# Kernel tuning notes

Measured on AMD Instinct MI355X. Metric: run time of the kernel, lower is better.

Reference implementation:

```python
import jax, jax.numpy as jnp
import numpy as np

VOCAB = 32000
D = 512
H = 8
B = 1
SEQ = 4096
CHUNK = 1024  # max_len == chunk size


def _pe(seq, d):
    pos = np.arange(seq, dtype=np.float32)[:, None]
    div = np.exp(np.arange(0, d, 2, dtype=np.float32) * (-np.log(10000.0) / d))
    pe = np.zeros((seq, d), dtype=np.float32)
    pe[:, 0::2] = np.sin(pos * div)
    pe[:, 1::2] = np.cos(pos * div)
    return jnp.asarray(pe)


def _mha(x, w_in, b_in, w_out, b_out, h):
    # x: (..., L, d); attention along L, batched over leading dims.
    lead = x.shape[:-2]
    L, d = x.shape[-2], x.shape[-1]
    hd = d // h
    qkv = x @ w_in.T + b_in                      # (..., L, 3d)
    q, k, v = jnp.split(qkv, 3, axis=-1)
    q = q.reshape(lead + (L, h, hd))
    k = k.reshape(lead + (L, h, hd))
    v = v.reshape(lead + (L, h, hd))
    scores = jnp.einsum('...qhd,...khd->...hqk', q, k) * (1.0 / np.sqrt(hd))
    attn = jax.nn.softmax(scores, axis=-1)
    o = jnp.einsum('...hqk,...khd->...qhd', attn, v).reshape(lead + (L, d))
    return o @ w_out.T + b_out


def _ln(x, g, b, eps=1e-5):
    m = x.mean(-1, keepdims=True)
    v = x.var(-1, keepdims=True)
    return (x - m) / jnp.sqrt(v + eps) * g + b


def setup_inputs() -> dict:
    key = jax.random.key(0)
    ks = jax.random.split(key, 10)
    n = lambda k, s: jax.random.normal(k, s, jnp.float32) * 0.02
    return {
        'tokens': jax.random.randint(ks[0], (B, SEQ), 0, VOCAB),
        'emb': n(ks[1], (VOCAB, D)),
        'chunk_w_in': n(ks[2], (3 * D, D)), 'chunk_b_in': jnp.zeros((3 * D,), jnp.float32),
        'chunk_w_out': n(ks[3], (D, D)), 'chunk_b_out': jnp.zeros((D,), jnp.float32),
        'glob_w_in': n(ks[4], (3 * D, D)), 'glob_b_in': jnp.zeros((3 * D,), jnp.float32),
        'glob_w_out': n(ks[5], (D, D)), 'glob_b_out': jnp.zeros((D,), jnp.float32),
        'ln1_g': jnp.ones((D,), jnp.float32), 'ln1_b': jnp.zeros((D,), jnp.float32),
        'ffn_w1': n(ks[6], (4 * D, D)), 'ffn_b1': jnp.zeros((4 * D,), jnp.float32),
        'ffn_w2': n(ks[7], (D, 4 * D)), 'ffn_b2': jnp.zeros((D,), jnp.float32),
        'ln2_g': jnp.ones((D,), jnp.float32), 'ln2_b': jnp.zeros((D,), jnp.float32),
        'fc_w': n(ks[8], (VOCAB, D)), 'fc_b': jnp.zeros((VOCAB,), jnp.float32),
    }


def reference(tokens, emb, chunk_w_in, chunk_b_in, chunk_w_out, chunk_b_out,
              glob_w_in, glob_b_in, glob_w_out, glob_b_out,
              ln1_g, ln1_b, ffn_w1, ffn_b1, ffn_w2, ffn_b2,
              ln2_g, ln2_b, fc_w, fc_b):
    # embedding * sqrt(d) + sinusoidal positional encoding (dropout in eval = identity)
    x = emb[tokens] * np.sqrt(D).astype(np.float32) + _pe(SEQ, D)[None]  # (B, S, d)
    b, s, d = x.shape
    nc = s // CHUNK
    # BeamSplitter chunk stage: attend across the nc chunks at each intra-chunk position
    xc = x.reshape(b, nc, CHUNK, d).transpose(0, 2, 1, 3)   # (B, CHUNK, nc, d)
    ca = _mha(xc, chunk_w_in, chunk_b_in, chunk_w_out, chunk_b_out, H)
    ca = ca.transpose(0, 2, 1, 3).reshape(b, s, d)          # (B, S, d)
    # global stage: full attention over the sequence
    ga = _mha(ca, glob_w_in, glob_b_in, glob_w_out, glob_b_out, H)
    # post-norm transformer encoder layer
    x = _ln(x + ga, ln1_g, ln1_b)
    f = jax.nn.relu(x @ ffn_w1.T + ffn_b1) @ ffn_w2.T + ffn_b2
    x = _ln(x + f, ln2_g, ln2_b)
    return x @ fc_w.T + fc_b                                 # (B, S, VOCAB)
```

## Files before the change

### kernel.cpp

```cpp
#include <hip/hip_runtime.h>

typedef __attribute__((ext_vector_type(8))) short bf16x8;
typedef __attribute__((ext_vector_type(4))) float f32x4;
typedef unsigned short u16;

__device__ __forceinline__ u16 f2b(float f) {
  union { float f; unsigned u; } v; v.f = f;
  return (u16)((v.u + 0x7FFFu + ((v.u >> 16) & 1u)) >> 16);
}
__device__ __forceinline__ float b2f(u16 x) {
  union { unsigned u; float f; } v; v.u = (unsigned)x << 16; return v.f;
}

__device__ __forceinline__ void gload16(const void* g, void* l) {
  __builtin_amdgcn_global_load_lds((__attribute__((address_space(1))) void*)(g),
                                   (__attribute__((address_space(3))) void*)(l),
                                   16, 0, 0);
}

__device__ __forceinline__ void mbar() {
  asm volatile("" ::: "memory");
  __builtin_amdgcn_s_barrier();
  asm volatile("" ::: "memory");
}

__device__ __forceinline__ void cv1(const float4* __restrict__ s, u16* __restrict__ d, int i) {
  float4 v = s[i];
  unsigned long long pk = (unsigned long long)f2b(v.x) |
                          ((unsigned long long)f2b(v.y) << 16) |
                          ((unsigned long long)f2b(v.z) << 32) |
                          ((unsigned long long)f2b(v.w) << 48);
  *(unsigned long long*)(d + (size_t)i * 4) = pk;
}

__global__ __launch_bounds__(256)
void prep(const int* __restrict__ tok, const float* __restrict__ emb,
          float* __restrict__ xf, u16* __restrict__ xb,
          const float4* s0, u16* d0, const float4* s1, u16* d1,
          const float4* s2, u16* d2, const float4* s3, u16* d3,
          const float4* s4, u16* d4, const float4* s5, u16* d5,
          const float4* s6, u16* d6) {
  if (blockIdx.x < 4096) {
    const int s = blockIdx.x;
    const int i = threadIdx.x;
    const int t = tok[s];
    const float div = __expf((float)(2 * i) * -0.017988946039015984f);
    const float ang = (float)s * div;
    const float sv = __sinf(ang), cv = __cosf(ang);
    const float* e = emb + (size_t)t * 512 + 2 * i;
    const float x0 = e[0] * 22.627416997969522f + sv;
    const float x1 = e[1] * 22.627416997969522f + cv;
    const size_t o = (size_t)s * 512 + 2 * i;
    xf[o] = x0; xf[o + 1] = x1;
    xb[o] = f2b(x0); xb[o + 1] = f2b(x1);
    return;
  }
  int i = (blockIdx.x - 4096) * 256 + threadIdx.x;
  const int stride = ((int)gridDim.x - 4096) * 256;
  for (; i < 5144576; i += stride) {
    int j = i;
    if (j < 196608) { cv1(s0, d0, j); continue; }
    j -= 196608;
    if (j < 65536) { cv1(s1, d1, j); continue; }
    j -= 65536;
    if (j < 196608) { cv1(s2, d2, j); continue; }
    j -= 196608;
    if (j < 65536) { cv1(s3, d3, j); continue; }
    j -= 65536;
    if (j < 262144) { cv1(s4, d4, j); continue; }
    j -= 262144;
    if (j < 262144) { cv1(s5, d5, j); continue; }
    j -= 262144;
    cv1(s6, d6, j);
  }
}

template<int BM, int BN, int RELU, int WF32, int WB16>
__global__ __launch_bounds__(256)
void gemm_bt(const u16* __restrict__ A, const u16* __restrict__ B,
             const float* __restrict__ bias, float* __restrict__ Cf,
             u16* __restrict__ Cb, int M, int N, int K)
{
  constexpr int MFR = BM / 32;
  constexpr int NFR = BN / 32;
  constexpr int INFLT = BM / 32 + BN / 32;
  __shared__ __align__(16) u16 As[2][BM * 64];
  __shared__ __align__(16) u16 Bs[2][BN * 64];
  const int tid = threadIdx.x;
  const int wid = tid >> 6, lane = tid & 63;
  const int lo = lane & 15, hi = lane >> 4;
  const int nbn = N / BN;
  const int cpx = (int)gridDim.x >> 3;
  const int bid = blockIdx.x;
  const int swz = (bid & 7) * cpx + (bid >> 3);
  const int bi = swz / nbn, bj = swz - bi * nbn;
  const size_t row0 = (size_t)bi * BM, col0 = (size_t)bj * BN;
  const int wr = (wid >> 1) * (BM / 2), wc = (wid & 1) * (BN / 2);
  const int srow = (wid << 3) + (lane >> 3);
  const int scol = ((lane & 7) ^ (lane >> 3)) << 3;

  f32x4 acc[MFR][NFR] = {};

  auto stage = [&](int t, int b) {
    const int k0 = t << 6;
#pragma unroll
    for (int p = 0; p < BM / 32; ++p)
      gload16(A + (row0 + srow + 32 * p) * (size_t)K + k0 + scol, &As[b][(wid * 8 + 32 * p) * 64]);
#pragma unroll
    for (int p = 0; p < BN / 32; ++p)
      gload16(B + (col0 + srow + 32 * p) * (size_t)K + k0 + scol, &Bs[b][(wid * 8 + 32 * p) * 64]);
  };

  auto rdf = [&](const u16* base, int row, int ks) -> bf16x8 {
    return *(const bf16x8*)((const char*)base + row * 128 + ((((ks << 2) | hi) ^ (row & 7)) << 4));
  };

  const int T = K >> 6;
  stage(0, 0);
  stage(1, 1);

  for (int t = 0; t < T; ++t) {
    if (t + 1 < T) {
      if constexpr (INFLT == 4)      { asm volatile("s_waitcnt vmcnt(4)" ::: "memory"); }
      else if constexpr (INFLT == 6) { asm volatile("s_waitcnt vmcnt(6)" ::: "memory"); }
      else                           { asm volatile("s_waitcnt vmcnt(8)" ::: "memory"); }
    } else {
      asm volatile("s_waitcnt vmcnt(0)" ::: "memory");
    }
    __builtin_amdgcn_sched_barrier(0);
    mbar();
    const u16* Ab = As[t & 1];
    const u16* Bb = Bs[t & 1];
#pragma unroll
    for (int ks = 0; ks < 2; ++ks) {
      bf16x8 af[MFR], bfr[NFR];
#pragma unroll
      for (int m = 0; m < MFR; ++m) af[m] = rdf(Ab, wr + m * 16 + lo, ks);
#pragma unroll
      for (int n = 0; n < NFR; ++n) bfr[n] = rdf(Bb, wc + n * 16 + lo, ks);
#pragma unroll
      for (int m = 0; m < MFR; ++m)
#pragma unroll
        for (int n = 0; n < NFR; ++n)
          acc[m][n] = __builtin_amdgcn_mfma_f32_16x16x32_bf16(af[m], bfr[n], acc[m][n], 0, 0, 0);
    }
    mbar();
    if (t + 2 < T) stage(t + 2, t & 1);
  }

#pragma unroll
  for (int m = 0; m < MFR; ++m)
#pragma unroll
    for (int n = 0; n < NFR; ++n) {
      const size_t c = col0 + wc + n * 16 + lo;
      const float bv = bias[c];
#pragma unroll
      for (int i = 0; i < 4; ++i) {
        const size_t r = row0 + wr + m * 16 + hi * 4 + i;
        float v = acc[m][n][i] + bv;
        if (RELU) v = fmaxf(v, 0.0f);
        if (WF32) Cf[r * (size_t)N + c] = v;
        if (WB16) Cb[r * (size_t)N + c] = f2b(v);
      }
    }
}

template<int KC>
__global__ __launch_bounds__(512, 2)
void gemm256(const u16* __restrict__ A, const u16* __restrict__ B,
             const float* __restrict__ bias, float* __restrict__ C,
             int M, int N)
{
  constexpr int T = KC / 64;
  __shared__ __align__(16) u16 LA[2][256 * 64];
  __shared__ __align__(16) u16 LB[2][256 * 64];
  const int tid = threadIdx.x;
  const int wid = tid >> 6, lane = tid & 63;
  const int lo = lane & 15, hi = lane >> 4;
  const int nbn = N >> 8;
  const int cpx = (int)gridDim.x >> 3;
  const int bid = blockIdx.x;
  const int swz = (bid & 7) * cpx + (bid >> 3);
  const int bi = swz / nbn, bj = swz - bi * nbn;
  const size_t row0 = (size_t)bi << 8, col0 = (size_t)bj << 8;
  const int wrow = (wid >> 2) << 7;
  const int wcol = (wid & 3) << 6;

  const int srow = (wid << 3) + (lane >> 3);
  const int scol = ((lane & 7) ^ (lane >> 3)) << 3;
  const u16* srcA = A + (row0 + srow) * (size_t)KC + scol;
  const u16* srcB = B + (col0 + srow) * (size_t)KC + scol;
  const int ldst = wid << 9;

  f32x4 acc[8][4] = {};

  auto stage = [&](int t, int b) {
    const size_t ko = (size_t)t * 64;
#pragma unroll
    for (int i = 0; i < 4; ++i)
      gload16(srcA + ko + (size_t)(i * 64) * KC, &LA[b][ldst + i * 4096]);
#pragma unroll
    for (int i = 0; i < 4; ++i)
      gload16(srcB + ko + (size_t)(i * 64) * KC, &LB[b][ldst + i * 4096]);
  };

  auto rd = [&](const u16* base, int row, int ks) -> bf16x8 {
    const int byte = row * 128 + ((((ks << 2) | hi) ^ (row & 7)) << 4);
    return *(const bf16x8*)((const char*)base + byte);
  };

  auto storeHalf = [&](int mbase) {
#pragma unroll
    for (int m = 0; m < 4; ++m)
#pragma unroll
      for (int n = 0; n < 4; ++n) {
        const size_t c = col0 + wcol + n * 16 + lo;
        const float bv = bias[c];
#pragma unroll
        for (int i = 0; i < 4; ++i) {
          const size_t r = row0 + wrow + (mbase + m) * 16 + hi * 4 + i;
          __builtin_nontemporal_store(acc[mbase + m][n][i] + bv, &C[r * (size_t)N + c]);
        }
      }
  };

  stage(0, 0);
  stage(1, 1);

  for (int t = 0; t < T - 1; ++t) {
    const int b = t & 1;
    const u16* Ab = LA[b];
    const u16* Bb = LB[b];
    asm volatile("s_waitcnt vmcnt(8)" ::: "memory");
    __builtin_amdgcn_sched_barrier(0);
    mbar();

    bf16x8 afr[4], bfr[4];
#pragma unroll
    for (int ks = 0; ks < 2; ++ks) {
#pragma unroll
      for (int m = 0; m < 4; ++m) afr[m] = rd(Ab, wrow + m * 16 + lo, ks);
#pragma unroll
      for (int n = 0; n < 4; ++n) bfr[n] = rd(Bb, wcol + n * 16 + lo, ks);
      mbar();
      asm volatile("s_waitcnt lgkmcnt(0)" ::: "memory");
      __builtin_amdgcn_sched_barrier(0);
      __builtin_amdgcn_s_setprio(1);
#pragma unroll
      for (int m = 0; m < 4; ++m)
#pragma unroll
        for (int n = 0; n < 4; ++n)
          acc[m][n] = __builtin_amdgcn_mfma_f32_16x16x32_bf16(afr[m], bfr[n], acc[m][n], 0, 0, 0);
      __builtin_amdgcn_s_setprio(0);
      mbar();
#pragma unroll
      for (int m = 0; m < 4; ++m) afr[m] = rd(Ab, wrow + (4 + m) * 16 + lo, ks);
      mbar();
      asm volatile("s_waitcnt lgkmcnt(0)" ::: "memory");
      __builtin_amdgcn_sched_barrier(0);
      __builtin_amdgcn_s_setprio(1);
#pragma unroll
      for (int m = 0; m < 4; ++m)
#pragma unroll
        for (int n = 0; n < 4; ++n)
          acc[4 + m][n] = __builtin_amdgcn_mfma_f32_16x16x32_bf16(afr[m], bfr[n], acc[4 + m][n], 0, 0, 0);
      __builtin_amdgcn_s_setprio(0);
      mbar();
    }
    if (t + 2 < T) stage(t + 2, b);
  }

  {
    const u16* Ab = LA[(T - 1) & 1];
    const u16* Bb = LB[(T - 1) & 1];
    asm volatile("s_waitcnt vmcnt(0)" ::: "memory");
    __builtin_amdgcn_sched_barrier(0);
    mbar();

    bf16x8 afr[4], bfr[4];
#pragma unroll
    for (int m = 0; m < 4; ++m) afr[m] = rd(Ab, wrow + m * 16 + lo, 0);
#pragma unroll
    for (int n = 0; n < 4; ++n) bfr[n] = rd(Bb, wcol + n * 16 + lo, 0);
    mbar();
    asm volatile("s_waitcnt lgkmcnt(0)" ::: "memory");
    __builtin_amdgcn_sched_barrier(0);
#pragma unroll
    for (int m = 0; m < 4; ++m)
#pragma unroll
      for (int n = 0; n < 4; ++n)
        acc[m][n] = __builtin_amdgcn_mfma_f32_16x16x32_bf16(afr[m], bfr[n], acc[m][n], 0, 0, 0);
    mbar();
#pragma unroll
    for (int m = 0; m < 4; ++m) afr[m] = rd(Ab, wrow + (4 + m) * 16 + lo, 0);
    mbar();
    asm volatile("s_waitcnt lgkmcnt(0)" ::: "memory");
    __builtin_amdgcn_sched_barrier(0);
#pragma unroll
    for (int m = 0; m < 4; ++m)
#pragma unroll
      for (int n = 0; n < 4; ++n)
        acc[4 + m][n] = __builtin_amdgcn_mfma_f32_16x16x32_bf16(afr[m], bfr[n], acc[4 + m][n], 0, 0, 0);
    mbar();
#pragma unroll
    for (int m = 0; m < 4; ++m) afr[m] = rd(Ab, wrow + m * 16 + lo, 1);
#pragma unroll
    for (int n = 0; n < 4; ++n) bfr[n] = rd(Bb, wcol + n * 16 + lo, 1);
    asm volatile("s_waitcnt lgkmcnt(0)" ::: "memory");
    __builtin_amdgcn_sched_barrier(0);
#pragma unroll
    for (int m = 0; m < 4; ++m)
#pragma unroll
      for (int n = 0; n < 4; ++n)
        acc[m][n] = __builtin_amdgcn_mfma_f32_16x16x32_bf16(afr[m], bfr[n], acc[m][n], 0, 0, 0);
    storeHalf(0);
#pragma unroll
    for (int m = 0; m < 4; ++m) afr[m] = rd(Ab, wrow + (4 + m) * 16 + lo, 1);
    asm volatile("s_waitcnt lgkmcnt(0)" ::: "memory");
    __builtin_amdgcn_sched_barrier(0);
#pragma unroll
    for (int m = 0; m < 4; ++m)
#pragma unroll
      for (int n = 0; n < 4; ++n)
        acc[4 + m][n] = __builtin_amdgcn_mfma_f32_16x16x32_bf16(afr[m], bfr[n], acc[4 + m][n], 0, 0, 0);
    storeHalf(4);
  }
}

__global__ __launch_bounds__(256)
void chunk_attn(const u16* __restrict__ qkv, u16* __restrict__ out) {
  const int widx = threadIdx.x >> 6, d = threadIdx.x & 63;
  const int g = blockIdx.x * 4 + widx;
  const int p = g & 1023, h = g >> 10;
  float q[4], k[4], v[4];
#pragma unroll
  for (int c = 0; c < 4; ++c) {
    const u16* b = qkv + (size_t)((c << 10) + p) * 1536 + (h << 6) + d;
    q[c] = b2f(b[0]); k[c] = b2f(b[512]); v[c] = b2f(b[1024]);
  }
  float sc[4][4];
#pragma unroll
  for (int i = 0; i < 4; ++i)
#pragma unroll
    for (int j = 0; j < 4; ++j) sc[i][j] = q[i] * k[j];
#pragma unroll
  for (int mask = 1; mask < 64; mask <<= 1)
#pragma unroll
    for (int i = 0; i < 4; ++i)
#pragma unroll
      for (int j = 0; j < 4; ++j) sc[i][j] += __shfl_xor(sc[i][j], mask);
#pragma unroll
  for (int i = 0; i < 4; ++i) {
    float s0 = sc[i][0] * 0.125f, s1 = sc[i][1] * 0.125f,
          s2 = sc[i][2] * 0.125f, s3 = sc[i][3] * 0.125f;
    const float mx = fmaxf(fmaxf(s0, s1), fmaxf(s2, s3));
    const float e0 = __expf(s0 - mx), e1 = __expf(s1 - mx),
                e2 = __expf(s2 - mx), e3 = __expf(s3 - mx);
    const float inv = 1.0f / (e0 + e1 + e2 + e3);
    const float o = (e0 * v[0] + e1 * v[1] + e2 * v[2] + e3 * v[3]) * inv;
    out[(size_t)((i << 10) + p) * 512 + (h << 6) + d] = f2b(o);
  }
}

__global__ __launch_bounds__(512, 4)
void flash_attn(const u16* __restrict__ qkv, float* __restrict__ pO,
                float* __restrict__ pm, float* __restrict__ pl) {
  __shared__ __align__(16) u16 Ks[64 * 64];
  __shared__ __align__(16) u16 Vt[64 * 64];
  __shared__ __align__(16) u16 Pp[8][16 * 64];
  const int tid = threadIdx.x, wid = tid >> 6, lane = tid & 63;
  const int lo = lane & 15, hi = lane >> 4;
  const int q0 = blockIdx.x << 7, h = blockIdx.y, z = blockIdx.z;
  const int kvb = z << 11;
  const int hoff = h << 6;
  char* KsB = (char*)Ks; char* VtB = (char*)Vt;
  char* Pw = (char*)&Pp[wid][0];
  const int xsw = (lo & 7) << 4;
  constexpr float C1 = 0.18033688011112042f;

  bf16x8 qf[2];
#pragma unroll
  for (int kh = 0; kh < 2; ++kh)
    qf[kh] = *(const bf16x8*)(qkv + (size_t)(q0 + wid * 16 + lo) * 1536 + hoff + kh * 32 + hi * 8);

  f32x4 o[4] = {};
  float mr = -3e38f, lr = 0.f;

  const int krow = tid >> 3, kq = tid & 7;

  bf16x8 kpre = *(const bf16x8*)(qkv + (size_t)(kvb + krow) * 1536 + 512 + hoff + kq * 8);
  bf16x8 vpre = *(const bf16x8*)(qkv + (size_t)(kvb + krow) * 1536 + 1024 + hoff + kq * 8);

  for (int kv0 = kvb; kv0 < kvb + 2048; kv0 += 64) {
    __syncthreads();
    *(bf16x8*)(KsB + ((krow * 128 + kq * 16) ^ ((krow & 7) << 4))) = kpre;
    {
      const unsigned* vp = (const unsigned*)&vpre;
      const int oddr = krow & 1;
      const unsigned t0 = oddr ? vp[0] : vp[2];
      const unsigned t1 = oddr ? vp[1] : vp[3];
      const unsigned r0 = (unsigned)__shfl_xor((int)t0, 8);
      const unsigned r1 = (unsigned)__shfl_xor((int)t1, 8);
      const unsigned E0 = oddr ? r0 : vp[0];
      const unsigned E1 = oddr ? r1 : vp[1];
      const unsigned O0 = oddr ? vp[2] : r0;
      const unsigned O1 = oddr ? vp[3] : r1;
      const int jp = krow & ~1;
      const int db = kq * 8 + oddr * 4;
      unsigned w0 = (E0 & 0xffffu) | (O0 << 16);
      unsigned w1 = (E0 >> 16) | (O0 & 0xffff0000u);
      unsigned w2 = (E1 & 0xffffu) | (O1 << 16);
      unsigned w3 = (E1 >> 16) | (O1 & 0xffff0000u);
      *(unsigned*)(VtB + (((db + 0) * 128 + 2 * jp) ^ (((db + 0) & 7) << 4))) = w0;
      *(unsigned*)(VtB + (((db + 1) * 128 + 2 * jp) ^ (((db + 1) & 7) << 4))) = w1;
      *(unsigned*)(VtB + (((db + 2) * 128 + 2 * jp) ^ (((db + 2) & 7) << 4))) = w2;
      *(unsigned*)(VtB + (((db + 3) * 128 + 2 * jp) ^ (((db + 3) & 7) << 4))) = w3;
    }
    __syncthreads();
    if (kv0 + 64 < kvb + 2048) {
      kpre = *(const bf16x8*)(qkv + (size_t)(kv0 + 64 + krow) * 1536 + 512 + hoff + kq * 8);
      vpre = *(const bf16x8*)(qkv + (size_t)(kv0 + 64 + krow) * 1536 + 1024 + hoff + kq * 8);
    }

    f32x4 s[4] = {};
#pragma unroll
    for (int n = 0; n < 4; ++n) {
      const int key = n * 16 + lo;
#pragma unroll
      for (int kh = 0; kh < 2; ++kh) {
        bf16x8 kf = *(const bf16x8*)(KsB + ((key * 128 + kh * 64 + hi * 16) ^ ((key & 7) << 4)));
        s[n] = __builtin_amdgcn_mfma_f32_16x16x32_bf16(kf, qf[kh], s[n], 0, 0, 0);
      }
    }

    float pmx = s[0][0];
#pragma unroll
    for (int n = 0; n < 4; ++n)
#pragma unroll
      for (int i = 0; i < 4; ++i) pmx = fmaxf(pmx, s[n][i]);
    pmx = fmaxf(pmx, __shfl_xor(pmx, 16));
    pmx = fmaxf(pmx, __shfl_xor(pmx, 32));

    if (__any(pmx > mr + 64.f)) {
      const float mn = fmaxf(mr, pmx);
      const float sc = exp2f((mr - mn) * C1);
      mr = mn;
      lr *= sc;
#pragma unroll
      for (int i = 0; i < 4; ++i) {
        const float sq = __shfl(sc, hi * 4 + i);
#pragma unroll
        for (int n = 0; n < 4; ++n) o[n][i] *= sq;
      }
    }

    const float mc = mr * C1;
    float rs = 0.f;
    unsigned U[8];
#pragma unroll
    for (int n = 0; n < 4; ++n) {
      const float p0 = exp2f(fmaf(s[n][0], C1, -mc));
      const float p1 = exp2f(fmaf(s[n][1], C1, -mc));
      const float p2 = exp2f(fmaf(s[n][2], C1, -mc));
      const float p3 = exp2f(fmaf(s[n][3], C1, -mc));
      rs += (p0 + p1) + (p2 + p3);
      asm("v_cvt_pk_bf16_f32 %0, %1, %2" : "=v"(U[2 * n])     : "v"(p0), "v"(p1));
      asm("v_cvt_pk_bf16_f32 %0, %1, %2" : "=v"(U[2 * n + 1]) : "v"(p2), "v"(p3));
    }
    rs += __shfl_xor(rs, 16);
    rs += __shfl_xor(rs, 32);
    lr += rs;
#pragma unroll
    for (int n = 0; n < 4; ++n) {
      const int off = lo * 128 + ((n * 32 + hi * 8) ^ xsw);
      const unsigned long long dw = (unsigned long long)U[2 * n] |
                                    ((unsigned long long)U[2 * n + 1] << 32);
      *(unsigned long long*)(Pw + off) = dw;
    }

#pragma unroll
    for (int kh = 0; kh < 2; ++kh) {
      bf16x8 pa = *(const bf16x8*)(Pw + lo * 128 + ((kh * 64 + hi * 16) ^ xsw));
#pragma unroll
      for (int n = 0; n < 4; ++n) {
        const int vd = n * 16 + lo;
        bf16x8 vf = *(const bf16x8*)(VtB + ((vd * 128 + kh * 64 + hi * 16) ^ ((vd & 7) << 4)));
        o[n] = __builtin_amdgcn_mfma_f32_16x16x32_bf16(pa, vf, o[n], 0, 0, 0);
      }
    }
  }

#pragma unroll
  for (int i = 0; i < 4; ++i) {
    const int r = q0 + wid * 16 + hi * 4 + i;
#pragma unroll
    for (int n = 0; n < 4; ++n)
      pO[((size_t)z * 4096 + r) * 512 + hoff + n * 16 + lo] = o[n][i];
  }
  if (hi == 0) {
    const int r = q0 + wid * 16 + lo;
    pm[(z * 8 + h) * 4096 + r] = mr;
    pl[(z * 8 + h) * 4096 + r] = lr;
  }
}

__global__ __launch_bounds__(256)
void attn_merge(const float* __restrict__ pO, const float* __restrict__ pm,
                const float* __restrict__ pl, u16* __restrict__ out) {
  constexpr float C1 = 0.18033688011112042f;
  const int tid = threadIdx.x, lane = tid & 63, w = tid >> 6;
  const int row = blockIdx.x * 4 + w;
  const int d = lane * 8, h = lane >> 3;
  const float m0 = pm[h * 4096 + row], m1 = pm[(8 + h) * 4096 + row];
  const float l0 = pl[h * 4096 + row], l1 = pl[(8 + h) * 4096 + row];
  const float M = fmaxf(m0, m1);
  const float w0 = exp2f((m0 - M) * C1), w1 = exp2f((m1 - M) * C1);
  const float inv = 1.0f / (l0 * w0 + l1 * w1);
  const float* a = pO + (size_t)row * 512 + d;
  const float* b = pO + ((size_t)4096 + row) * 512 + d;
  float4 a0 = *(const float4*)a, a1 = *(const float4*)(a + 4);
  float4 b0 = *(const float4*)b, b1 = *(const float4*)(b + 4);
  const float A[8] = {a0.x, a0.y, a0.z, a0.w, a1.x, a1.y, a1.z, a1.w};
  const float Bv[8] = {b0.x, b0.y, b0.z, b0.w, b1.x, b1.y, b1.z, b1.w};
#pragma unroll
  for (int j = 0; j < 8; ++j)
    out[(size_t)row * 512 + d + j] = f2b((A[j] * w0 + Bv[j] * w1) * inv);
}

template<int WF32>
__global__ __launch_bounds__(256)
void add_ln(const float* __restrict__ a, const float* __restrict__ b,
            const float* __restrict__ g, const float* __restrict__ be,
            float* __restrict__ of, u16* __restrict__ ob) {
  const int wid = threadIdx.x >> 6, lane = threadIdx.x & 63;
  const int row = blockIdx.x * 4 + wid;
  const size_t base = (size_t)row * 512 + lane * 8;
  float4 a0 = *(const float4*)(a + base), a1 = *(const float4*)(a + base + 4);
  float4 b0 = *(const float4*)(b + base), b1 = *(const float4*)(b + base + 4);
  float x[8] = {a0.x + b0.x, a0.y + b0.y, a0.z + b0.z, a0.w + b0.w,
                a1.x + b1.x, a1.y + b1.y, a1.z + b1.z, a1.w + b1.w};
  float s = 0.f, sq = 0.f;
#pragma unroll
  for (int j = 0; j < 8; ++j) { s += x[j]; sq += x[j] * x[j]; }
#pragma unroll
  for (int mask = 1; mask < 64; mask <<= 1) {
    s += __shfl_xor(s, mask);
    sq += __shfl_xor(sq, mask);
  }
  const float mean = s * (1.0f / 512.0f);
  const float var = sq * (1.0f / 512.0f) - mean * mean;
  const float rstd = rsqrtf(var + 1e-5f);
  float4 g0 = *(const float4*)(g + lane * 8), g1 = *(const float4*)(g + lane * 8 + 4);
  float4 e0 = *(const float4*)(be + lane * 8), e1 = *(const float4*)(be + lane * 8 + 4);
  const float gg[8] = {g0.x, g0.y, g0.z, g0.w, g1.x, g1.y, g1.z, g1.w};
  const float bb[8] = {e0.x, e0.y, e0.z, e0.w, e1.x, e1.y, e1.z, e1.w};
#pragma unroll
  for (int j = 0; j < 8; ++j) {
    const float y = (x[j] - mean) * rstd * gg[j] + bb[j];
    if (WF32) of[base + j] = y;
    ob[base + j] = f2b(y);
  }
}

extern "C" void kernel_launch(void* const* d_in, const int* in_sizes, int n_in,
                              void* d_out, int out_size, void* d_ws, size_t ws_size,
                              hipStream_t stream) {
  (void)in_sizes; (void)n_in; (void)out_size; (void)ws_size;
  const int*   tokens = (const int*)d_in[0];
  const float* emb    = (const float*)d_in[1];
  const float* cwin   = (const float*)d_in[2];
  const float* cbin   = (const float*)d_in[3];
  const float* cwout  = (const float*)d_in[4];
  const float* cbout  = (const float*)d_in[5];
  const float* gwin   = (const float*)d_in[6];
  const float* gbin   = (const float*)d_in[7];
  const float* gwout  = (const float*)d_in[8];
  const float* gbout  = (const float*)d_in[9];
  const float* ln1g   = (const float*)d_in[10];
  const float* ln1b   = (const float*)d_in[11];
  const float* fw1    = (const float*)d_in[12];
  const float* fb1    = (const float*)d_in[13];
  const float* fw2    = (const float*)d_in[14];
  const float* fb2    = (const float*)d_in[15];
  const float* ln2g   = (const float*)d_in[16];
  const float* ln2b   = (const float*)d_in[17];
  const float* fcw    = (const float*)d_in[18];
  const float* fcb    = (const float*)d_in[19];
  float* out = (float*)d_out;

  char* ws = (char*)d_ws;
  size_t off = 0;
  auto alloc = [&](size_t bytes) -> void* {
    void* p = ws + off;
    off += (bytes + 255) & ~(size_t)255;
    return p;
  };
  u16*   xb    = (u16*)alloc((size_t)4096 * 512 * 2);
  float* xf    = (float*)alloc((size_t)4096 * 512 * 4);
  u16*   qkv1b = (u16*)alloc((size_t)4096 * 1536 * 2);
  u16*   at1   = (u16*)alloc((size_t)4096 * 512 * 2);
  u16*   cab   = (u16*)alloc((size_t)4096 * 512 * 2);
  u16*   qkv2  = (u16*)alloc((size_t)4096 * 1536 * 2);
  u16*   at2   = (u16*)alloc((size_t)4096 * 512 * 2);
  float* gaf   = (float*)alloc((size_t)4096 * 512 * 4);
  float* x1f   = (float*)alloc((size_t)4096 * 512 * 4);
  u16*   x1b   = (u16*)alloc((size_t)4096 * 512 * 2);
  u16*   f1b   = (u16*)alloc((size_t)4096 * 2048 * 2);
  float* ff    = (float*)alloc((size_t)4096 * 512 * 4);
  u16*   x2b   = (u16*)alloc((size_t)4096 * 512 * 2);
  u16*   wcinb  = (u16*)alloc((size_t)1536 * 512 * 2);
  u16*   wcoutb = (u16*)alloc((size_t)512 * 512 * 2);
  u16*   wginb  = (u16*)alloc((size_t)1536 * 512 * 2);
  u16*   wgoutb = (u16*)alloc((size_t)512 * 512 * 2);
  u16*   wf1b   = (u16*)alloc((size_t)2048 * 512 * 2);
  u16*   wf2b   = (u16*)alloc((size_t)512 * 2048 * 2);
  u16*   wfcb   = (u16*)alloc((size_t)32000 * 512 * 2);

  float* pO = (float*)qkv1b;
  float* pm = (float*)xb;
  float* pl = pm + 2 * 8 * 4096;

  prep<<<4096 + 2048, 256, 0, stream>>>(
      tokens, emb, xf, xb,
      (const float4*)cwin, wcinb, (const float4*)cwout, wcoutb,
      (const float4*)gwin, wginb, (const float4*)gwout, wgoutb,
      (const float4*)fw1, wf1b, (const float4*)fw2, wf2b,
      (const float4*)fcw, wfcb);

  gemm_bt<64, 128, 0, 0, 1><<<768, 256, 0, stream>>>(xb, wcinb, cbin, (float*)nullptr, qkv1b, 4096, 1536, 512);
  chunk_attn<<<2048, 256, 0, stream>>>(qkv1b, at1);
  gemm_bt<64, 64, 0, 0, 1><<<512, 256, 0, stream>>>(at1, wcoutb, cbout, (float*)nullptr, cab, 4096, 512, 512);

  gemm_bt<64, 128, 0, 0, 1><<<768, 256, 0, stream>>>(cab, wginb, gbin, (float*)nullptr, qkv2, 4096, 1536, 512);
  flash_attn<<<dim3(32, 8, 2), 512, 0, stream>>>(qkv2, pO, pm, pl);
  attn_merge<<<1024, 256, 0, stream>>>(pO, pm, pl, at2);
  gemm_bt<64, 64, 0, 1, 0><<<512, 256, 0, stream>>>(at2, wgoutb, gbout, gaf, (u16*)nullptr, 4096, 512, 512);

  add_ln<1><<<1024, 256, 0, stream>>>(xf, gaf, ln1g, ln1b, x1f, x1b);
  gemm_bt<64, 128, 1, 0, 1><<<1024, 256, 0, stream>>>(x1b, wf1b, fb1, (float*)nullptr, f1b, 4096, 2048, 512);
  gemm_bt<64, 64, 0, 1, 0><<<512, 256, 0, stream>>>(f1b, wf2b, fb2, ff, (u16*)nullptr, 4096, 512, 2048);
  add_ln<0><<<1024, 256, 0, stream>>>(x1f, ff, ln2g, ln2b, (float*)nullptr, x2b);

  gemm256<512><<<2000, 512, 0, stream>>>(x2b, wfcb, fcb, out, 4096, 32000);
}
```

Measured before the change: 426.6 us.

## Fold chunk-attention output projection into global QKV projection weights

Precomputes a fused weight W_glob_in · W_chunk_out (with a transposed bf16 copy of the chunk output weight and a folded bias) each call, so the chunk-attention output feeds straight into the global QKV GEMM. This removes one 4096x512x512 GEMM and the intermediate cab buffer write and read. In exchange it adds a small 1536x512x512 weight GEMM, a transpose/bias kernel and an extra launch. Rounding the fused weight to bf16 changes numerics slightly.

```diff
diff --git a/kernel.cpp b/kernel.cpp
--- a/kernel.cpp
+++ b/kernel.cpp
@@ -36,10 +36,9 @@
 __global__ __launch_bounds__(256)
 void prep(const int* __restrict__ tok, const float* __restrict__ emb,
           float* __restrict__ xf, u16* __restrict__ xb,
-          const float4* s0, u16* d0, const float4* s1, u16* d1,
-          const float4* s2, u16* d2, const float4* s3, u16* d3,
-          const float4* s4, u16* d4, const float4* s5, u16* d5,
-          const float4* s6, u16* d6) {
+          const float4* s0, u16* d0, const float4* s2, u16* d2,
+          const float4* s3, u16* d3, const float4* s4, u16* d4,
+          const float4* s5, u16* d5, const float4* s6, u16* d6) {
   if (blockIdx.x < 4096) {
     const int s = blockIdx.x;
     const int i = threadIdx.x;
@@ -57,12 +56,10 @@
   }
   int i = (blockIdx.x - 4096) * 256 + threadIdx.x;
   const int stride = ((int)gridDim.x - 4096) * 256;
-  for (; i < 5144576; i += stride) {
+  for (; i < 5079040; i += stride) {
     int j = i;
     if (j < 196608) { cv1(s0, d0, j); continue; }
     j -= 196608;
-    if (j < 65536) { cv1(s1, d1, j); continue; }
-    j -= 65536;
     if (j < 196608) { cv1(s2, d2, j); continue; }
     j -= 196608;
     if (j < 65536) { cv1(s3, d3, j); continue; }
@@ -72,6 +69,55 @@
     if (j < 262144) { cv1(s5, d5, j); continue; }
     j -= 262144;
     cv1(s6, d6, j);
+  }
+}
+
+__global__ __launch_bounds__(256)
+void tbz(const float* __restrict__ cwout, const float* __restrict__ gwin,
+         const float* __restrict__ cbout, const float* __restrict__ gbin,
+         u16* __restrict__ wcoutT, float* __restrict__ bp, float* __restrict__ zb) {
+  const int b = blockIdx.x;
+  if (b < 64) {
+    __shared__ float tile[64][65];
+    const int bi = b >> 3, bj = b & 7;
+    const int tr = threadIdx.x >> 2;
+    const int tc = (threadIdx.x & 3) << 4;
+    const float* src = cwout + (size_t)(bj * 64 + tr) * 512 + bi * 64 + tc;
+#pragma unroll
+    for (int q = 0; q < 4; ++q) {
+      float4 v = *(const float4*)(src + q * 4);
+      tile[tr][tc + q * 4 + 0] = v.x;
+      tile[tr][tc + q * 4 + 1] = v.y;
+      tile[tr][tc + q * 4 + 2] = v.z;
+      tile[tr][tc + q * 4 + 3] = v.w;
+    }
+    __syncthreads();
+    u16* dst = wcoutT + (size_t)(bi * 64 + tr) * 512 + bj * 64 + tc;
+#pragma unroll
+    for (int q = 0; q < 2; ++q) {
+      unsigned long long pk0 = 0, pk1 = 0;
+#pragma unroll
+      for (int e = 0; e < 4; ++e)
+        pk0 |= (unsigned long long)f2b(tile[tc + q * 8 + e][tr]) << (16 * e);
+#pragma unroll
+      for (int e = 0; e < 4; ++e)
+        pk1 |= (unsigned long long)f2b(tile[tc + q * 8 + 4 + e][tr]) << (16 * e);
+      *(unsigned long long*)(dst + q * 8) = pk0;
+      *(unsigned long long*)(dst + q * 8 + 4) = pk1;
+    }
+  } else {
+    const int i = (b - 64) * 256 + threadIdx.x;
+    if (i < 1536) {
+      float s = gbin[i];
+      const float4* wr = (const float4*)(gwin + (size_t)i * 512);
+      const float4* cb = (const float4*)cbout;
+      for (int k = 0; k < 128; ++k) {
+        float4 w = wr[k], c = cb[k];
+        s += w.x * c.x + w.y * c.y + w.z * c.z + w.w * c.w;
+      }
+      bp[i] = s;
+      if (i < 512) zb[i] = 0.f;
+    }
   }
 }
 
@@ -599,7 +645,6 @@
   float* xf    = (float*)alloc((size_t)4096 * 512 * 4);
   u16*   qkv1b = (u16*)alloc((size_t)4096 * 1536 * 2);
   u16*   at1   = (u16*)alloc((size_t)4096 * 512 * 2);
-  u16*   cab   = (u16*)alloc((size_t)4096 * 512 * 2);
   u16*   qkv2  = (u16*)alloc((size_t)4096 * 1536 * 2);
   u16*   at2   = (u16*)alloc((size_t)4096 * 512 * 2);
   float* gaf   = (float*)alloc((size_t)4096 * 512 * 4);
@@ -609,9 +654,12 @@
   float* ff    = (float*)alloc((size_t)4096 * 512 * 4);
   u16*   x2b   = (u16*)alloc((size_t)4096 * 512 * 2);
   u16*   wcinb  = (u16*)alloc((size_t)1536 * 512 * 2);
-  u16*   wcoutb = (u16*)alloc((size_t)512 * 512 * 2);
+  u16*   wcoutT = (u16*)alloc((size_t)512 * 512 * 2);
   u16*   wginb  = (u16*)alloc((size_t)1536 * 512 * 2);
   u16*   wgoutb = (u16*)alloc((size_t)512 * 512 * 2);
+  u16*   wfoldb = (u16*)alloc((size_t)1536 * 512 * 2);
+  float* bp     = (float*)alloc((size_t)1536 * 4);
+  float* zb     = (float*)alloc((size_t)512 * 4);
   u16*   wf1b   = (u16*)alloc((size_t)2048 * 512 * 2);
   u16*   wf2b   = (u16*)alloc((size_t)512 * 2048 * 2);
   u16*   wfcb   = (u16*)alloc((size_t)32000 * 512 * 2);
@@ -620,18 +668,20 @@
   float* pm = (float*)xb;
   float* pl = pm + 2 * 8 * 4096;
 
+  tbz<<<70, 256, 0, stream>>>(cwout, gwin, cbout, gbin, wcoutT, bp, zb);
+
   prep<<<4096 + 2048, 256, 0, stream>>>(
       tokens, emb, xf, xb,
-      (const float4*)cwin, wcinb, (const float4*)cwout, wcoutb,
-      (const float4*)gwin, wginb, (const float4*)gwout, wgoutb,
-      (const float4*)fw1, wf1b, (const float4*)fw2, wf2b,
-      (const float4*)fcw, wfcb);
+      (const float4*)cwin, wcinb, (const float4*)gwin, wginb,
+      (const float4*)gwout, wgoutb, (const float4*)fw1, wf1b,
+      (const float4*)fw2, wf2b, (const float4*)fcw, wfcb);
+
+  gemm_bt<64, 128, 0, 0, 1><<<96, 256, 0, stream>>>(wginb, wcoutT, zb, (float*)nullptr, wfoldb, 1536, 512, 512);
 
   gemm_bt<64, 128, 0, 0, 1><<<768, 256, 0, stream>>>(xb, wcinb, cbin, (float*)nullptr, qkv1b, 4096, 1536, 512);
   chunk_attn<<<2048, 256, 0, stream>>>(qkv1b, at1);
-  gemm_bt<64, 64, 0, 0, 1><<<512, 256, 0, stream>>>(at1, wcoutb, cbout, (float*)nullptr, cab, 4096, 512, 512);
-
-  gemm_bt<64, 128, 0, 0, 1><<<768, 256, 0, stream>>>(cab, wginb, gbin, (float*)nullptr, qkv2, 4096, 1536, 512);
+
+  gemm_bt<64, 128, 0, 0, 1><<<768, 256, 0, stream>>>(at1, wfoldb, bp, (float*)nullptr, qkv2, 4096, 1536, 512);
   flash_attn<<<dim3(32, 8, 2), 512, 0, stream>>>(qkv2, pO, pm, pl);
   attn_merge<<<1024, 256, 0, stream>>>(pO, pm, pl, at2);
   gemm_bt<64, 64, 0, 1, 0><<<512, 256, 0, stream>>>(at2, wgoutb, gbout, gaf, (u16*)nullptr, 4096, 512, 512);
```

After: 443.1 us. 3.9% more time.
